# Kernel optimization log

Measured on AMD Instinct MI355X. Metric: run time of the kernel, lower is better.

The kernel has to match this reference:

```python
import jax, jax.numpy as jnp
import numpy as np
from jax import lax

B, T, NI = 1024, 16, 11

def skew(v):  # [...,3,1] -> [...,3,3]
    x, y, z = v[..., 0, 0], v[..., 1, 0], v[..., 2, 0]
    o = jnp.zeros_like(x)
    return jnp.stack([jnp.stack([o, -z, y], -1),
                      jnp.stack([z, o, -x], -1),
                      jnp.stack([-y, x, o], -1)], -2)

def exp_SO3(phi):  # [...,3,1] -> [...,3,3] (Rodrigues, safe small-angle)
    t2 = jnp.sum(phi * phi, axis=(-2, -1))[..., None, None]
    small = t2 < 1e-8
    t2s = jnp.where(small, 1.0, t2)
    t = jnp.sqrt(t2s)
    A = jnp.where(small, 1.0 - t2 / 6.0, jnp.sin(t) / t)
    Bc = jnp.where(small, 0.5 - t2 / 24.0, (1.0 - jnp.cos(t)) / t2s)
    K = skew(phi)
    return jnp.eye(3, dtype=phi.dtype) + A * K + Bc * (K @ K)

def log_SO3(C):  # [...,3,3] -> [...,3,1]
    tr = jnp.trace(C, axis1=-2, axis2=-1)[..., None, None]
    c = jnp.clip((tr - 1.0) * 0.5, -1.0 + 1e-7, 1.0 - 1e-7)
    t = jnp.arccos(c)
    small = t < 1e-4
    s = jnp.where(small, 1.0, jnp.sin(t))
    coef = jnp.where(small, 0.5 + t * t / 12.0, t / (2.0 * s))
    S = coef * (C - jnp.swapaxes(C, -1, -2))
    return jnp.stack([S[..., 2, 1], S[..., 0, 2], S[..., 1, 0]], -1)[..., None]

def J_left_inv(phi):  # inverse left Jacobian of SO(3)
    t2 = jnp.sum(phi * phi, axis=(-2, -1))[..., None, None]
    small = t2 < 1e-8
    t2s = jnp.where(small, 1.0, t2)
    t = jnp.sqrt(t2s)
    coef = jnp.where(small, 1.0 / 12.0,
                     1.0 / t2s - (1.0 + jnp.cos(t)) / (2.0 * t * jnp.sin(t)))
    K = skew(phi)
    return jnp.eye(3, dtype=phi.dtype) - 0.5 * K + coef * (K @ K)

def decode(s):
    b = s.shape[0]
    return (s[:, 0:3].reshape(b, 3, 1), s[:, 3:12].reshape(b, 3, 3),
            s[:, 12:15].reshape(b, 3, 1), s[:, 15:18].reshape(b, 3, 1),
            s[:, 18:21].reshape(b, 3, 1), s[:, 21:24].reshape(b, 3, 1),
            s[:, 24].reshape(b, 1, 1))

def encode(g, C, r, v, bw, ba, lambd):
    b = g.shape[0]
    return jnp.concatenate([g.reshape(b, 3), C.reshape(b, 9), r.reshape(b, 3),
                            v.reshape(b, 3), bw.reshape(b, 3), ba.reshape(b, 3),
                            lambd.reshape(b, 1)], -1)

def force_sym(M):
    u = jnp.triu(M)
    return u + jnp.swapaxes(u, -1, -2) * (1.0 - jnp.eye(M.shape[-1], dtype=M.dtype))

def predict_one_step(t_acc, C_acc, r_acc, v_acc, dt, g_k, v_k, bw_k, ba_k, covar, gyro, accel, Rimu):
    b = dt.shape[0]
    dt2 = dt * dt
    w = gyro - bw_k
    w_sk = skew(w)
    C_T = jnp.swapaxes(C_acc, -1, -2)
    a = accel - ba_k
    v = C_T @ (v_k - g_k * t_acc + v_acc)
    v_sk = skew(v)
    I3 = jnp.eye(3, dtype=dt.dtype)
    E = exp_SO3(dt * w)
    E_T = jnp.swapaxes(E, -1, -2)
    F = jnp.zeros((b, 19, 19), dt.dtype)
    F = F.at[:, 3:6, 3:6].set(-w_sk)
    F = F.at[:, 3:6, 12:15].set(-I3)
    F = F.at[:, 6:9, 3:6].set(-(C_acc @ v_sk))
    F = F.at[:, 6:9, 9:12].set(C_acc)
    F = F.at[:, 9:12, 0:3].set(-C_T)
    F = F.at[:, 9:12, 3:6].set(-skew(C_T @ g_k))
    F = F.at[:, 9:12, 9:12].set(-w_sk)
    F = F.at[:, 9:12, 12:15].set(-v_sk)
    F = F.at[:, 9:12, 15:18].set(-I3)
    G = jnp.zeros((b, 19, 12), dt.dtype)
    G = G.at[:, 3:6, 0:3].set(-I3)
    G = G.at[:, 9:12, 0:3].set(-v_sk)
    G = G.at[:, 9:12, 6:9].set(-I3)
    G = G.at[:, 12:15, 3:6].set(I3)
    G = G.at[:, 15:18, 9:12].set(I3)
    Phi = jnp.eye(19, dtype=dt.dtype) + F * dt + 0.5 * (F @ F) * dt2
    Phi = Phi.at[:, 6:9, 12:15].set(0.0)
    Phi = Phi.at[:, 3:6, 3:6].set(E_T)
    Phi = Phi.at[:, 9:12, 9:12].set(E_T)
    PhiG = Phi @ G
    Q = (PhiG @ Rimu @ jnp.swapaxes(PhiG, -1, -2)) * dt
    covar = force_sym(Phi @ covar @ jnp.swapaxes(Phi, -1, -2) + Q)
    r_acc = r_acc + v_acc * dt + 0.5 * (C_acc @ (dt2 * a))
    v_acc = v_acc + C_acc @ (dt * a)
    C_acc = C_acc @ E
    t_acc = t_acc + dt
    return t_acc, C_acc, r_acc, v_acc, covar

def predict(imu_meas, Rimu, prev_state, prev_covar):
    b = imu_meas.shape[0]
    dtype = prev_covar.dtype
    g_k, _, _, v_k, bw_k, ba_k, lambd = decode(prev_state)
    u = jnp.array([1.0] * 3 + [0.0] * 6 + [1.0] * 10, dtype)
    covar = prev_covar * (u[:, None] * u[None, :])  # U P U^T with diagonal U
    t = imu_meas[..., 0]
    gyro = imu_meas[..., 1:4][..., None]
    accel = imu_meas[..., 4:7][..., None]
    dt = (t[:, 1:] - t[:, :-1])[..., None, None]
    init = (jnp.zeros((b, 1, 1), dtype),
            jnp.tile(jnp.eye(3, dtype=dtype), (b, 1, 1)),
            jnp.zeros((b, 3, 1), dtype), jnp.zeros((b, 3, 1), dtype), covar)
    xs = (jnp.swapaxes(dt, 0, 1), jnp.swapaxes(gyro[:, :-1], 0, 1), jnp.swapaxes(accel[:, :-1], 0, 1))
    def step(c, x):
        t_acc, C_acc, r_acc, v_acc, cov = c
        dt_, gy, ac = x
        return predict_one_step(t_acc, C_acc, r_acc, v_acc, dt_, g_k, v_k, bw_k, ba_k, cov, gy, ac, Rimu), None
    (t_acc, C_acc, r_acc, v_acc, cov), _ = lax.scan(step, init, xs)
    pred_state = encode(g_k, C_acc,
                        v_k * t_acc - 0.5 * g_k * t_acc * t_acc + r_acc,
                        jnp.swapaxes(C_acc, -1, -2) @ (v_k - g_k * t_acc + v_acc),
                        bw_k, ba_k, lambd)
    return pred_state, cov

def update(pred_state, pred_covar, vis_meas, vis_meas_covar):
    b = pred_state.shape[0]
    dtype = pred_state.dtype
    g_p, C_p, r_p, v_p, bw_p, ba_p, l_p = decode(pred_state)
    phi = log_SO3(C_p)
    residual = jnp.concatenate([vis_meas[:, 0:3] - phi, vis_meas[:, 3:6] - l_p * r_p], 1)
    H = jnp.zeros((b, 6, 19), dtype)
    H = H.at[:, 0:3, 3:6].set(-J_left_inv(-phi))
    H = H.at[:, 3:6, 6:9].set(-jnp.eye(3, dtype=dtype) * l_p)
    H = H.at[:, 3:6, 18:19].set(-r_p)
    H = -H
    H_T = jnp.swapaxes(H, -1, -2)
    S = H @ pred_covar @ H_T + vis_meas_covar
    K = pred_covar @ H_T @ jnp.linalg.inv(S)
    e = K @ residual
    est_covar = (jnp.eye(19, dtype=dtype) - K @ H) @ pred_covar
    est_state = encode(g_p + e[:, 0:3], C_p @ exp_SO3(e[:, 3:6]), r_p + e[:, 6:9],
                       v_p + e[:, 9:12], bw_p + e[:, 12:15], ba_p + e[:, 15:18],
                       l_p + e[:, 18:19])
    return est_state, est_covar

def composition(prev_pose, est_state, est_covar):
    b = est_state.shape[0]
    dtype = est_state.dtype
    g, C, r, v, bw, ba, lambd = decode(est_state)
    C_T = jnp.swapaxes(C, -1, -2)
    pose = jnp.tile(jnp.eye(4, dtype=dtype), (b, 1, 1))
    pose = pose.at[:, 0:3, 0:3].set(C_T @ prev_pose[:, 0:3, 0:3])
    pose = pose.at[:, 0:3, 3:4].set(C_T @ (prev_pose[:, 0:3, 3:4] - r))
    new_g = C_T @ g
    new_state = encode(new_g, C, r, v, bw, ba, lambd)
    U = jnp.tile(jnp.eye(19, dtype=dtype), (b, 1, 1))
    U = U.at[:, 0:3, 0:3].set(C_T)
    U = U.at[:, 0:3, 3:6].set(skew(new_g))
    new_covar = force_sym(U @ est_covar @ jnp.swapaxes(U, -1, -2))
    return pose, new_state, new_covar

def setup_inputs() -> dict:
    key = jax.random.key(0)
    k1, k2, k3 = jax.random.split(key, 3)
    dtype = jnp.float32
    times = jnp.broadcast_to(jnp.arange(NI, dtype=dtype) * 0.01, (B, T, NI))
    gyro = jax.random.normal(k1, (B, T, NI, 3), dtype) * 0.05
    accel = jax.random.normal(k2, (B, T, NI, 3), dtype) * 0.1
    imu_data = jnp.concatenate([times[..., None], gyro, accel], -1)  # [B,T,NI,7]
    imu_noise_covar = jnp.eye(12, dtype=dtype) * 1e-4
    prev_pose = jnp.tile(jnp.eye(4, dtype=dtype), (B, 1, 1))
    g0 = jnp.array([0.0, 0.0, 9.81], dtype)
    C0 = jnp.eye(3, dtype=dtype).reshape(9)
    prev_state = jnp.broadcast_to(
        jnp.concatenate([g0, C0, jnp.zeros(12, dtype), jnp.ones(1, dtype)]), (B, 25))
    prev_covar = jnp.tile(jnp.eye(19, dtype=dtype) * 1e-2, (B, 1, 1))
    vis_meas = jax.random.normal(k3, (B, T, 6, 1), dtype) * 0.01
    vis_meas_covar = jnp.tile(jnp.eye(6, dtype=dtype) * 1e-2, (B, T, 1, 1))
    T_imu_cam = jnp.tile(jnp.eye(4, dtype=dtype), (B, 1, 1))
    return dict(imu_data=imu_data, imu_noise_covar=imu_noise_covar, prev_pose=prev_pose,
                prev_state=prev_state, prev_covar=prev_covar, vis_meas=vis_meas,
                vis_meas_covar=vis_meas_covar, T_imu_cam=T_imu_cam)

def reference(imu_data, imu_noise_covar, prev_pose, prev_state, prev_covar, vis_meas, vis_meas_covar, T_imu_cam):
    num_timesteps = vis_meas.shape[1]
    poses, states, covars = [prev_pose], [prev_state], [prev_covar]
    for k in range(num_timesteps):
        ps, pc = predict(imu_data[:, k], imu_noise_covar, states[-1], covars[-1])
        es, ec = update(ps, pc, vis_meas[:, k], vis_meas_covar[:, k])
        npo, ns, nc = composition(poses[-1], es, ec)
        poses.append(npo); states.append(ns); covars.append(nc)
    return (jnp.stack(poses, 1), jnp.stack(states, 1), jnp.stack(covars, 1))
```

## Files before the change

### kernel.cpp

```cpp
#include <hip/hip_runtime.h>

#define NB 1024
#define NT 16
#define NIM 11
#define PIT 20
#define NTH 256
#define TPF 128

struct __align__(16) SharedBlob {
    float P0[19*PIT];
    float P1[19*PIT];
    float A9[9*PIT];
    float Dall[10][9*PIT];
    float W9[9*12];
    float Wr9[9*12];
    float Wu[19*12];
    float Mu[19*12];
    float T[3*PIT];
    float Rd[12];
    float Aug[2][84];
    float E[20];
    float vvs[10][4];
    float dts[12];
    unsigned short tri[192];
};

__device__ __forceinline__ float sel3(int i, float a, float b, float c){
    return i==0 ? a : (i==1 ? b : c);
}
__device__ __forceinline__ void skew3(float x, float y, float z, float K[9]) {
    K[0]=0.f;  K[1]=-z;   K[2]=y;
    K[3]=z;    K[4]=0.f;  K[5]=-x;
    K[6]=-y;   K[7]=x;    K[8]=0.f;
}
__device__ __forceinline__ void mm3(const float A[9], const float Bm[9], float C[9]) {
#pragma unroll
    for (int i=0;i<3;i++)
#pragma unroll
        for (int j=0;j<3;j++)
            C[i*3+j] = A[i*3+0]*Bm[0+j] + A[i*3+1]*Bm[3+j] + A[i*3+2]*Bm[6+j];
}
__device__ __forceinline__ void exp_SO3f(float p0, float p1, float p2, float R[9]) {
    float t2 = p0*p0+p1*p1+p2*p2;
    bool sm = t2 < 1e-8f;
    float t2s = sm ? 1.0f : t2;
    float t = sqrtf(t2s);
    float sn, cs; __sincosf(t, &sn, &cs);
    float A = sm ? (1.0f - t2*(1.0f/6.0f)) : (sn/t);
    float Bc = sm ? (0.5f - t2*(1.0f/24.0f)) : ((1.0f - cs)/t2s);
    float K[9]; skew3(p0,p1,p2,K);
    float K2[9]; mm3(K,K,K2);
#pragma unroll
    for (int i=0;i<9;i++) R[i] = A*K[i] + Bc*K2[i];
    R[0]+=1.f; R[4]+=1.f; R[8]+=1.f;
}
__device__ __forceinline__ void log_SO3(const float C[9], float p[3]) {
    float tr = C[0]+C[4]+C[8];
    float c = (tr-1.0f)*0.5f;
    c = fminf(fmaxf(c, -1.0f+1e-7f), 1.0f-1e-7f);
    float t = acosf(c);
    bool sm = t < 1e-4f;
    float s = sm ? 1.0f : sinf(t);
    float coef = sm ? (0.5f + t*t*(1.0f/12.0f)) : (t/(2.0f*s));
    p[0] = coef*(C[7]-C[5]);
    p[1] = coef*(C[2]-C[6]);
    p[2] = coef*(C[3]-C[1]);
}
__device__ __forceinline__ void J_left_inv(const float p[3], float J[9]) {
    float t2 = p[0]*p[0]+p[1]*p[1]+p[2]*p[2];
    bool sm = t2 < 1e-8f;
    float t2s = sm ? 1.0f : t2;
    float t = sqrtf(t2s);
    float coef = sm ? (1.0f/12.0f) : (1.0f/t2s - (1.0f+cosf(t))/(2.0f*t*sinf(t)));
    float K[9]; skew3(p[0],p[1],p[2],K);
    float K2[9]; mm3(K,K,K2);
#pragma unroll
    for (int i=0;i<9;i++) J[i] = -0.5f*K[i] + coef*K2[i];
    J[0]+=1.f; J[4]+=1.f; J[8]+=1.f;
}
__device__ __forceinline__ float dot19_rr(const float* a, const float* b){
    const float4* a4=(const float4*)a;
    const float4* b4=(const float4*)b;
    float s=0.f;
#pragma unroll
    for (int q=0;q<4;q++){
        float4 x=a4[q], y=b4[q];
        s += x.x*y.x + x.y*y.y + x.z*y.z + x.w*y.w;
    }
    s += a[16]*b[16]+a[17]*b[17]+a[18]*b[18];
    return s;
}
__device__ __forceinline__ float dot12_rr(const float* a, const float* b){
    const float4* a4=(const float4*)a;
    const float4* b4=(const float4*)b;
    float s=0.f;
#pragma unroll
    for (int q=0;q<3;q++){
        float4 x=a4[q], y=b4[q];
        s += x.x*y.x + x.y*y.y + x.z*y.z + x.w*y.w;
    }
    return s;
}

__global__ void __launch_bounds__(NTH, 2) kf_kernel(
    const float* __restrict__ imu_data,
    const float* __restrict__ Rimu,
    const float* __restrict__ prev_pose,
    const float* __restrict__ prev_state,
    const float* __restrict__ prev_covar,
    const float* __restrict__ vis_meas,
    const float* __restrict__ vis_covar,
    float* __restrict__ out_poses,
    float* __restrict__ out_states,
    float* __restrict__ out_covars)
{
    __shared__ SharedBlob SS[2];
    const int tid = threadIdx.x;
    const int f   = tid >> 7;
    const int t   = tid & (TPF-1);
    const int b   = blockIdx.x*2 + f;
    SharedBlob& S = SS[f];

    const float* pcv = prev_covar + (size_t)b*361;
    for (int e=t;e<361;e+=TPF){
        float v = pcv[e];
        int i=e/19, j=e%19;
        bool msk = (i>=3&&i<9)||(j>=3&&j<9);
        S.P0[i*PIT + j] = msk ? 0.f : v;
        out_covars[((size_t)b*17)*361 + e] = v;
    }
    for (int e=t;e<10*9*PIT;e+=TPF) S.Dall[0][e] = 0.f;
    if (t<12) S.Rd[t] = Rimu[t*12+t];
    if (t<16) out_poses[((size_t)b*17)*16 + t] = prev_pose[(size_t)b*16+t];
    if (t<25) out_states[((size_t)b*17)*25 + t] = prev_state[(size_t)b*25+t];
    for (int e=t;e<190;e+=TPF){
        int i=0, rem=e;
        while (rem >= 19-i){ rem -= 19-i; i++; }
        S.tri[e] = (unsigned short)((i<<5)|(i+rem));
    }

    const float* st = prev_state + (size_t)b*25;
    float g0=st[0], g1=st[1], g2=st[2];
    float vk0=st[15], vk1=st[16], vk2=st[17];
    float bw0=st[18], bw1=st[19], bw2=st[20];
    float ba0=st[21], ba1=st[22], ba2=st[23];
    float lam=st[24];
    const float* pp = prev_pose + (size_t)b*16;
    float pR[9] = {pp[0],pp[1],pp[2], pp[4],pp[5],pp[6], pp[8],pp[9],pp[10]};
    float pT0=pp[3], pT1=pp[7], pT2=pp[11];

    __syncthreads();

    for (int k=0;k<NT;k++){
        float Cc[9] = {1,0,0, 0,1,0, 0,0,1};
        float ra0=0,ra1=0,ra2=0, va0=0,va1=0,va2=0, tac=0;
        const float* imu = imu_data + ((size_t)b*NT + k)*NIM*7;

        for (int s=0;s<NIM-1;s++){
            const float* m0 = imu + s*7;
            float dt = m0[7] - m0[0];
            float w0=m0[1]-bw0, w1=m0[2]-bw1, w2=m0[3]-bw2;
            float a0=m0[4]-ba0, a1=m0[5]-ba1, a2=m0[6]-ba2;
            float u0=vk0-g0*tac+va0, u1=vk1-g1*tac+va1, u2=vk2-g2*tac+va2;
            float vv0=Cc[0]*u0+Cc[3]*u1+Cc[6]*u2;
            float vv1=Cc[1]*u0+Cc[4]*u1+Cc[7]*u2;
            float vv2=Cc[2]*u0+Cc[5]*u1+Cc[8]*u2;
            float ct0=Cc[0]*g0+Cc[3]*g1+Cc[6]*g2;
            float ct1=Cc[1]*g0+Cc[4]*g1+Cc[7]*g2;
            float ct2=Cc[2]*g0+Cc[5]*g1+Cc[8]*g2;
            float Em[9]; exp_SO3f(dt*w0, dt*w1, dt*w2, Em);
            float hdt2 = 0.5f*dt*dt;

            if (t<27){
                int r=t/9, ii=(t%9)/3, jj=t%3;
                float dij = (ii==jj)?1.f:0.f;
                int o = ii*PIT + jj;
                float* Dp = S.Dall[s];
                if (r==0){
                    float eJ0=sel3(jj,Em[0],Em[3],Em[6]), eJ1=sel3(jj,Em[1],Em[4],Em[7]), eJ2=sel3(jj,Em[2],Em[5],Em[8]);
                    float EmTIJ = sel3(ii,eJ0,eJ1,eJ2);
                    float wcJ0=sel3(jj,0.f,-w2,w1), wcJ1=sel3(jj,w2,0.f,-w0), wcJ2=sel3(jj,-w1,w0,0.f);
                    float wskIJ = sel3(ii,wcJ0,wcJ1,wcJ2);
                    Dp[o+3]  = EmTIJ - dij;
                    Dp[o+12] = -dt*dij + hdt2*wskIJ;
                } else if (r==1){
                    float cI0=sel3(ii,Cc[0],Cc[3],Cc[6]), cI1=sel3(ii,Cc[1],Cc[4],Cc[7]), cI2=sel3(ii,Cc[2],Cc[5],Cc[8]);
                    float cJ0=sel3(jj,Cc[0],Cc[3],Cc[6]), cJ1=sel3(jj,Cc[1],Cc[4],Cc[7]), cJ2=sel3(jj,Cc[2],Cc[5],Cc[8]);
                    float ccJ0=sel3(jj,Cc[0],Cc[1],Cc[2]), ccJ1=sel3(jj,Cc[3],Cc[4],Cc[5]), ccJ2=sel3(jj,Cc[6],Cc[7],Cc[8]);
                    float CIJ = sel3(ii,ccJ0,ccJ1,ccJ2);
                    float vcJ0=sel3(jj,0.f,-vv2,vv1), vcJ1=sel3(jj,vv2,0.f,-vv0), vcJ2=sel3(jj,-vv1,vv0,0.f);
                    float tcJ0=sel3(jj,0.f,-ct2,ct1), tcJ1=sel3(jj,ct2,0.f,-ct0), tcJ2=sel3(jj,-ct1,ct0,0.f);
                    float wcJ0=sel3(jj,0.f,-w2,w1), wcJ1=sel3(jj,w2,0.f,-w0), wcJ2=sel3(jj,-w1,w0,0.f);
                    float CCtIJ  = cI0*cJ0 + cI1*cJ1 + cI2*cJ2;
                    float CvskIJ = cI0*vcJ0 + cI1*vcJ1 + cI2*vcJ2;
                    float Cv0 =  cI1*vv2 - cI2*vv1;
                    float Cv1 = -cI0*vv2 + cI2*vv0;
                    float Cv2 =  cI0*vv1 - cI1*vv0;
                    float CvwIJ = Cv0*wcJ0 + Cv1*wcJ1 + Cv2*wcJ2;
                    float CctIJ = cI0*tcJ0 + cI1*tcJ1 + cI2*tcJ2;
                    float CwIJ  = cI0*wcJ0 + cI1*wcJ1 + cI2*wcJ2;
                    Dp[3*PIT + o + 0]  = -hdt2*CCtIJ;
                    Dp[3*PIT + o + 3]  = -dt*CvskIJ + hdt2*(CvwIJ - CctIJ);
                    Dp[3*PIT + o + 9]  =  dt*CIJ - hdt2*CwIJ;
                    Dp[3*PIT + o + 15] = -hdt2*CIJ;
                } else {
                    float cJ0=sel3(jj,Cc[0],Cc[3],Cc[6]), cJ1=sel3(jj,Cc[1],Cc[4],Cc[7]), cJ2=sel3(jj,Cc[2],Cc[5],Cc[8]);
                    float CTIJ = sel3(ii,cJ0,cJ1,cJ2);
                    float eJ0=sel3(jj,Em[0],Em[3],Em[6]), eJ1=sel3(jj,Em[1],Em[4],Em[7]), eJ2=sel3(jj,Em[2],Em[5],Em[8]);
                    float EmTIJ = sel3(ii,eJ0,eJ1,eJ2);
                    float wrI0=sel3(ii,0.f,w2,-w1), wrI1=sel3(ii,-w2,0.f,w0), wrI2=sel3(ii,w1,-w0,0.f);
                    float wcJ0=sel3(jj,0.f,-w2,w1), wcJ1=sel3(jj,w2,0.f,-w0), wcJ2=sel3(jj,-w1,w0,0.f);
                    float wskIJ = sel3(ii,wcJ0,wcJ1,wcJ2);
                    float vcJ0=sel3(jj,0.f,-vv2,vv1), vcJ1=sel3(jj,vv2,0.f,-vv0), vcJ2=sel3(jj,-vv1,vv0,0.f);
                    float vskIJ = sel3(ii,vcJ0,vcJ1,vcJ2);
                    float trI0=sel3(ii,0.f,ct2,-ct1), trI1=sel3(ii,-ct2,0.f,ct0), trI2=sel3(ii,ct1,-ct0,0.f);
                    float tcJ0=sel3(jj,0.f,-ct2,ct1), tcJ1=sel3(jj,ct2,0.f,-ct0), tcJ2=sel3(jj,-ct1,ct0,0.f);
                    float ctskIJ = sel3(ii,tcJ0,tcJ1,tcJ2);
                    float wCtIJ = wrI0*cJ0 + wrI1*cJ1 + wrI2*cJ2;
                    float ctwIJ = trI0*wcJ0 + trI1*wcJ1 + trI2*wcJ2;
                    float wctIJ = wrI0*tcJ0 + wrI1*tcJ1 + wrI2*tcJ2;
                    float wvIJ  = wrI0*vcJ0 + wrI1*vcJ1 + wrI2*vcJ2;
                    Dp[6*PIT + o + 0]  = -dt*CTIJ + hdt2*wCtIJ;
                    Dp[6*PIT + o + 3]  = -dt*ctskIJ + hdt2*(ctwIJ + wctIJ);
                    Dp[6*PIT + o + 9]  = EmTIJ - dij;
                    Dp[6*PIT + o + 12] = -dt*vskIJ + hdt2*(ctskIJ + wvIJ);
                    Dp[6*PIT + o + 15] = -dt*dij + hdt2*wskIJ;
                }
            }
            if (t<3) S.vvs[s][t] = sel3(t, vv0, vv1, vv2);
            if (t==3) S.dts[s] = dt;

            float d2 = dt*dt;
            float e0=d2*a0, e1=d2*a1, e2=d2*a2;
            ra0 += va0*dt + 0.5f*(Cc[0]*e0+Cc[1]*e1+Cc[2]*e2);
            ra1 += va1*dt + 0.5f*(Cc[3]*e0+Cc[4]*e1+Cc[5]*e2);
            ra2 += va2*dt + 0.5f*(Cc[6]*e0+Cc[7]*e1+Cc[8]*e2);
            float da0=dt*a0, da1=dt*a1, da2=dt*a2;
            va0 += Cc[0]*da0+Cc[1]*da1+Cc[2]*da2;
            va1 += Cc[3]*da0+Cc[4]*da1+Cc[5]*da2;
            va2 += Cc[6]*da0+Cc[7]*da1+Cc[8]*da2;
            float Cn[9]; mm3(Cc, Em, Cn);
#pragma unroll
            for (int q=0;q<9;q++) Cc[q]=Cn[q];
            tac += dt;
        }
        __syncthreads();

        for (int s=0;s<NIM-1;s++){
            float* Pc = (s&1) ? S.P1 : S.P0;
            float* Pn = (s&1) ? S.P0 : S.P1;
            const float* Ds = S.Dall[s];
            float vv0=S.vvs[s][0], vv1=S.vvs[s][1], vv2=S.vvs[s][2];
            float dt = S.dts[s];

            for (int e=t;e<279;e+=TPF){
                if (e<171){
                    int i=e/19, j=e%19;
                    const float* Dr = &Ds[i*PIT];
                    float s2 = Pc[(3+i)*PIT+j]
                             + Dr[0]*Pc[0*PIT+j]+Dr[1]*Pc[1*PIT+j]+Dr[2]*Pc[2*PIT+j]
                             + Dr[3]*Pc[3*PIT+j]+Dr[4]*Pc[4*PIT+j]+Dr[5]*Pc[5*PIT+j]
                             + Dr[9]*Pc[9*PIT+j]+Dr[10]*Pc[10*PIT+j]+Dr[11]*Pc[11*PIT+j]
                             + Dr[12]*Pc[12*PIT+j]+Dr[13]*Pc[13*PIT+j]+Dr[14]*Pc[14*PIT+j]
                             + Dr[15]*Pc[15*PIT+j]+Dr[16]*Pc[16*PIT+j]+Dr[17]*Pc[17*PIT+j];
                    S.A9[i*PIT+j]=s2;
                } else {
                    int e2=e-171; int i=e2/12, j=e2%12;
                    const float* Dr = &Ds[i*PIT];
                    int ri = 3+i;
                    float val;
                    if (j<3){
                        float v0j = sel3(j, 0.f, -vv2,  vv1);
                        float v1j = sel3(j, vv2,  0.f, -vv0);
                        float v2j = sel3(j,-vv1,  vv0,  0.f);
                        val = -((ri==3+j)?1.f:0.f) - Dr[3+j]
                              - (((ri==9 )?1.f:0.f)+Dr[9 ])*v0j
                              - (((ri==10)?1.f:0.f)+Dr[10])*v1j
                              - (((ri==11)?1.f:0.f)+Dr[11])*v2j;
                    } else if (j<6) val = Dr[9+j];
                    else if (j<9) val = -(((ri==j+3)?1.f:0.f) + Dr[j+3]);
                    else val = Dr[6+j];
                    S.W9[i*12+j]=val;
                    S.Wr9[i*12+j]=val*S.Rd[j];
                }
            }
            __syncthreads();

            for (int e=t;e<190;e+=TPF){
                int tt=S.tri[e]; int i=tt>>5, j=tt&31;
                const float* Ai = (i>=3 && i<12) ? &S.A9[(i-3)*PIT] : &Pc[i*PIT];
                float val = Ai[j];
                if (j>=3 && j<12) val += dot19_rr(Ai, &Ds[(j-3)*PIT]);
                if (i>=3){
                    if (j<12) val += dt*dot12_rr(&S.Wr9[(i-3)*12], &S.W9[(j-3)*12]);
                    else if (i<12){
                        if (j<15) val += dt*S.Wr9[(i-3)*12 + (j-9)];
                        else if (j<18) val += dt*S.Wr9[(i-3)*12 + (j-6)];
                    } else if (i==j){
                        if (i<15) val += dt*S.Rd[i-9];
                        else if (i<18) val += dt*S.Rd[i-6];
                    }
                }
                Pn[i*PIT+j]=val; Pn[j*PIT+i]=val;
            }
            __syncthreads();
        }

        float t2a = tac*tac;
        float rp0 = vk0*tac - 0.5f*g0*t2a + ra0;
        float rp1 = vk1*tac - 0.5f*g1*t2a + ra1;
        float rp2 = vk2*tac - 0.5f*g2*t2a + ra2;
        float u0=vk0-g0*tac+va0, u1=vk1-g1*tac+va1, u2=vk2-g2*tac+va2;
        float vpr0=Cc[0]*u0+Cc[3]*u1+Cc[6]*u2;
        float vpr1=Cc[1]*u0+Cc[4]*u1+Cc[7]*u2;
        float vpr2=Cc[2]*u0+Cc[5]*u1+Cc[8]*u2;

        float phi[3]; log_SO3(Cc, phi);
        float nphi[3]={-phi[0],-phi[1],-phi[2]};
        float Jli[9]; J_left_inv(nphi, Jli);
        const float* vm = vis_meas + ((size_t)b*NT+k)*6;
        float res0=vm[0]-phi[0], res1=vm[1]-phi[1], res2=vm[2]-phi[2];
        float res3=vm[3]-lam*rp0, res4=vm[4]-lam*rp1, res5=vm[5]-lam*rp2;

        if (t<114){
            int i=t/6, j=t%6;
            float val;
            if (j<3){
                float jr0 = sel3(j, Jli[0], Jli[3], Jli[6]);
                float jr1 = sel3(j, Jli[1], Jli[4], Jli[7]);
                float jr2 = sel3(j, Jli[2], Jli[5], Jli[8]);
                val = S.P0[i*PIT+3]*jr0 + S.P0[i*PIT+4]*jr1 + S.P0[i*PIT+5]*jr2;
            } else {
                float rsel = sel3(j-3, rp0, rp1, rp2);
                val = lam*S.P0[i*PIT+6+(j-3)] + rsel*S.P0[i*PIT+18];
            }
            S.Wu[i*12+j]=val;
        }
        __syncthreads();
        const float* vmc = vis_covar + ((size_t)b*NT+k)*36;
        if (t<84){
            int i=t/14, c=t%14;
            float val;
            if (c<6){
                float hp;
                if (i<3){
                    float jr0 = sel3(i, Jli[0], Jli[3], Jli[6]);
                    float jr1 = sel3(i, Jli[1], Jli[4], Jli[7]);
                    float jr2 = sel3(i, Jli[2], Jli[5], Jli[8]);
                    hp = jr0*S.Wu[3*12+c]+jr1*S.Wu[4*12+c]+jr2*S.Wu[5*12+c];
                } else {
                    float rsel = sel3(i-3, rp0, rp1, rp2);
                    hp = lam*S.Wu[(3+i)*12+c] + rsel*S.Wu[18*12+c];
                }
                val = hp + vmc[i*6+c];
            } else val = ((c-6)==i)?1.f:0.f;
            S.Aug[0][i*14+c]=val;
        }
        __syncthreads();
        if (t<64){
            int i0=t/14, c0=t%14;
            int e1=t+64, i1=e1/14, c1=e1%14;
            bool h1 = e1<84;
            int cur=0;
#pragma unroll
            for (int kk=0;kk<6;kk++){
                const float* Ac = S.Aug[cur];
                float* An = S.Aug[cur^1];
                float rpv = 1.0f/Ac[kk*14+kk];
                float piv0 = Ac[kk*14+c0]*rpv;
                float nv0 = (i0==kk)? piv0 : (Ac[i0*14+c0] - Ac[i0*14+kk]*piv0);
                float nv1 = 0.f;
                if (h1){
                    float piv1 = Ac[kk*14+c1]*rpv;
                    nv1 = (i1==kk)? piv1 : (Ac[i1*14+c1] - Ac[i1*14+kk]*piv1);
                }
                An[i0*14+c0]=nv0;
                if (h1) An[i1*14+c1]=nv1;
                cur^=1;
                __builtin_amdgcn_wave_barrier();
            }
        }
        __syncthreads();
        if (t<114){
            int i=t/6, j=t%6;
            float s2=0.f;
#pragma unroll
            for (int m=0;m<6;m++) s2 += S.Wu[i*12+m]*S.Aug[0][m*14+6+j];
            S.Mu[i*12+j]=s2;
        }
        __syncthreads();
        for (int e=t;e<133;e+=TPF){
            int i=e/7, c=e%7;
            float val;
            if (c<3){
                float jc0 = sel3(c, Jli[0], Jli[1], Jli[2]);
                float jc1 = sel3(c, Jli[3], Jli[4], Jli[5]);
                float jc2 = sel3(c, Jli[6], Jli[7], Jli[8]);
                val = S.Mu[i*12+0]*jc0 + S.Mu[i*12+1]*jc1 + S.Mu[i*12+2]*jc2;
            }
            else if (c<6) val = S.Mu[i*12+c]*lam;
            else val = S.Mu[i*12+3]*rp0 + S.Mu[i*12+4]*rp1 + S.Mu[i*12+5]*rp2;
            S.Wu[i*12+c]=val;
        }
        if (t<19){
            S.E[t] = S.Mu[t*12+0]*res0 + S.Mu[t*12+1]*res1 + S.Mu[t*12+2]*res2
                   + S.Mu[t*12+3]*res3 + S.Mu[t*12+4]*res4 + S.Mu[t*12+5]*res5;
        }
        __syncthreads();
        for (int e=t;e<361;e+=TPF){
            int i=e/19, j=e%19;
            float s2 = S.P0[i*PIT+j];
#pragma unroll
            for (int c=0;c<6;c++) s2 -= S.Wu[i*12+c]*S.P0[(3+c)*PIT+j];
            s2 -= S.Wu[i*12+6]*S.P0[18*PIT+j];
            S.P1[i*PIT+j]=s2;
        }
        float ev[19];
#pragma unroll
        for (int q=0;q<19;q++) ev[q]=S.E[q];
        g0+=ev[0]; g1+=ev[1]; g2+=ev[2];
        float dE[9]; exp_SO3f(ev[3], ev[4], ev[5], dE);
        float Ce[9]; mm3(Cc,dE,Ce);
        float re0=rp0+ev[6], re1=rp1+ev[7], re2=rp2+ev[8];
        float vE0=vpr0+ev[9], vE1=vpr1+ev[10], vE2=vpr2+ev[11];
        bw0+=ev[12]; bw1+=ev[13]; bw2+=ev[14];
        ba0+=ev[15]; ba1+=ev[16]; ba2+=ev[17];
        lam+=ev[18];
        float gn0=Ce[0]*g0+Ce[3]*g1+Ce[6]*g2;
        float gn1=Ce[1]*g0+Ce[4]*g1+Ce[7]*g2;
        float gn2=Ce[2]*g0+Ce[5]*g1+Ce[8]*g2;
        float Rn[9];
#pragma unroll
        for (int i=0;i<3;i++)
#pragma unroll
            for (int j=0;j<3;j++)
                Rn[i*3+j] = Ce[0*3+i]*pR[0*3+j] + Ce[1*3+i]*pR[1*3+j] + Ce[2*3+i]*pR[2*3+j];
        float dv0=pT0-re0, dv1=pT1-re1, dv2=pT2-re2;
        float Tn0=Ce[0]*dv0+Ce[3]*dv1+Ce[6]*dv2;
        float Tn1=Ce[1]*dv0+Ce[4]*dv1+Ce[7]*dv2;
        float Tn2=Ce[2]*dv0+Ce[5]*dv1+Ce[8]*dv2;
        __syncthreads();
        if (t<57){
            int i=t/19, j=t%19;
            float c0 = sel3(i, Ce[0], Ce[1], Ce[2]);
            float c1 = sel3(i, Ce[3], Ce[4], Ce[5]);
            float c2 = sel3(i, Ce[6], Ce[7], Ce[8]);
            float gs0 = sel3(i, 0.f,  gn2, -gn1);
            float gs1 = sel3(i, -gn2, 0.f,  gn0);
            float gs2 = sel3(i, gn1, -gn0,  0.f);
            float val = c0*S.P1[0*PIT+j] + c1*S.P1[1*PIT+j] + c2*S.P1[2*PIT+j]
                      + gs0*S.P1[3*PIT+j] + gs1*S.P1[4*PIT+j] + gs2*S.P1[5*PIT+j];
            S.T[i*PIT+j]=val;
        }
        __syncthreads();
        size_t obase = (size_t)b*17 + (size_t)(k+1);
        for (int e=t;e<190;e+=TPF){
            int tt=S.tri[e]; int i=tt>>5, j=tt&31;
            float val;
            if (j<3){
                float c0 = sel3(j, Ce[0], Ce[1], Ce[2]);
                float c1 = sel3(j, Ce[3], Ce[4], Ce[5]);
                float c2 = sel3(j, Ce[6], Ce[7], Ce[8]);
                float gs0 = sel3(j, 0.f,  gn2, -gn1);
                float gs1 = sel3(j, -gn2, 0.f,  gn0);
                float gs2 = sel3(j, gn1, -gn0,  0.f);
                val = S.T[i*PIT+0]*c0 + S.T[i*PIT+1]*c1 + S.T[i*PIT+2]*c2
                    + S.T[i*PIT+3]*gs0 + S.T[i*PIT+4]*gs1 + S.T[i*PIT+5]*gs2;
            } else {
                val = (i<3) ? S.T[i*PIT+j] : S.P1[i*PIT+j];
            }
            bool msk = (i>=3&&i<9)||(j>=3&&j<9);
            float pv = msk ? 0.f : val;
            S.P0[i*PIT+j]=pv; S.P0[j*PIT+i]=pv;
            out_covars[obase*361 + i*19 + j] = val;
            if (i!=j) out_covars[obase*361 + j*19 + i] = val;
        }
        if (t==0){
            float* po = out_poses + obase*16;
            po[0]=Rn[0]; po[1]=Rn[1]; po[2]=Rn[2];  po[3]=Tn0;
            po[4]=Rn[3]; po[5]=Rn[4]; po[6]=Rn[5];  po[7]=Tn1;
            po[8]=Rn[6]; po[9]=Rn[7]; po[10]=Rn[8]; po[11]=Tn2;
            po[12]=0.f; po[13]=0.f; po[14]=0.f; po[15]=1.f;
            float* so = out_states + obase*25;
            so[0]=gn0; so[1]=gn1; so[2]=gn2;
#pragma unroll
            for (int q=0;q<9;q++) so[3+q]=Ce[q];
            so[12]=re0; so[13]=re1; so[14]=re2;
            so[15]=vE0; so[16]=vE1; so[17]=vE2;
            so[18]=bw0; so[19]=bw1; so[20]=bw2;
            so[21]=ba0; so[22]=ba1; so[23]=ba2;
            so[24]=lam;
        }
        g0=gn0; g1=gn1; g2=gn2;
        vk0=vE0; vk1=vE1; vk2=vE2;
#pragma unroll
        for (int q=0;q<9;q++) pR[q]=Rn[q];
        pT0=Tn0; pT1=Tn1; pT2=Tn2;
        __syncthreads();
    }
}

extern "C" void kernel_launch(void* const* d_in, const int* in_sizes, int n_in,
                              void* d_out, int out_size, void* d_ws, size_t ws_size,
                              hipStream_t stream) {
    const float* imu    = (const float*)d_in[0];
    const float* Rimu   = (const float*)d_in[1];
    const float* ppose  = (const float*)d_in[2];
    const float* pstate = (const float*)d_in[3];
    const float* pcov   = (const float*)d_in[4];
    const float* vm     = (const float*)d_in[5];
    const float* vmc    = (const float*)d_in[6];
    float* out = (float*)d_out;
    float* out_poses  = out;
    float* out_states = out + (size_t)NB*17*16;
    float* out_covars = out + (size_t)NB*17*16 + (size_t)NB*17*25;
    hipLaunchKernelGGL(kf_kernel, dim3(NB/2), dim3(NTH), 0, stream,
        imu, Rimu, ppose, pstate, pcov, vm, vmc, out_poses, out_states, out_covars);
}
```

Baseline: 676.0 us.

## Hoist W construction into the propagation loop and split covariance work per wave

The per-step W/Wr matrices are now built in the first propagation loop by wave 0 and stored for all steps. They use a sqrt(Rd) symmetric scaling, so a single array serves both dot-product operands. In the covariance recursion the A9 product and the upper-triangle update are split between the two waves along their data dependencies, which replaces one block-wide __syncthreads per step with wave-local barriers. The trade-off is more shared memory (10 stored W matrices) and an uneven work split between waves. It also assumes Dall[s] is visible to wave 0 without a block barrier, and that the Rd entries are non-negative for sqrt.

```diff
diff --git a/kernel.cpp b/kernel.cpp
--- a/kernel.cpp
+++ b/kernel.cpp
@@ -12,15 +12,14 @@
     float P1[19*PIT];
     float A9[9*PIT];
     float Dall[10][9*PIT];
-    float W9[9*12];
-    float Wr9[9*12];
+    float Wsall[10][9*12];
     float Wu[19*12];
     float Mu[19*12];
     float T[3*PIT];
     float Rd[12];
+    float sqRd[12];
     float Aug[2][84];
     float E[20];
-    float vvs[10][4];
     float dts[12];
     unsigned short tri[192];
 };
@@ -120,6 +119,8 @@
     const int t   = tid & (TPF-1);
     const int b   = blockIdx.x*2 + f;
     SharedBlob& S = SS[f];
+    const int w = t >> 6;
+    const int l = t & 63;
 
     const float* pcv = prev_covar + (size_t)b*361;
     for (int e=t;e<361;e+=TPF){
@@ -130,7 +131,7 @@
         out_covars[((size_t)b*17)*361 + e] = v;
     }
     for (int e=t;e<10*9*PIT;e+=TPF) S.Dall[0][e] = 0.f;
-    if (t<12) S.Rd[t] = Rimu[t*12+t];
+    if (t<12){ float rv = Rimu[t*12+t]; S.Rd[t]=rv; S.sqRd[t]=sqrtf(rv); }
     if (t<16) out_poses[((size_t)b*17)*16 + t] = prev_pose[(size_t)b*16+t];
     if (t<25) out_states[((size_t)b*17)*25 + t] = prev_state[(size_t)b*25+t];
     for (int e=t;e<190;e+=TPF){
@@ -227,46 +228,16 @@
                     Dp[6*PIT + o + 15] = -dt*dij + hdt2*wskIJ;
                 }
             }
-            if (t<3) S.vvs[s][t] = sel3(t, vv0, vv1, vv2);
             if (t==3) S.dts[s] = dt;
-
-            float d2 = dt*dt;
-            float e0=d2*a0, e1=d2*a1, e2=d2*a2;
-            ra0 += va0*dt + 0.5f*(Cc[0]*e0+Cc[1]*e1+Cc[2]*e2);
-            ra1 += va1*dt + 0.5f*(Cc[3]*e0+Cc[4]*e1+Cc[5]*e2);
-            ra2 += va2*dt + 0.5f*(Cc[6]*e0+Cc[7]*e1+Cc[8]*e2);
-            float da0=dt*a0, da1=dt*a1, da2=dt*a2;
-            va0 += Cc[0]*da0+Cc[1]*da1+Cc[2]*da2;
-            va1 += Cc[3]*da0+Cc[4]*da1+Cc[5]*da2;
-            va2 += Cc[6]*da0+Cc[7]*da1+Cc[8]*da2;
-            float Cn[9]; mm3(Cc, Em, Cn);
-#pragma unroll
-            for (int q=0;q<9;q++) Cc[q]=Cn[q];
-            tac += dt;
-        }
-        __syncthreads();
-
-        for (int s=0;s<NIM-1;s++){
-            float* Pc = (s&1) ? S.P1 : S.P0;
-            float* Pn = (s&1) ? S.P0 : S.P1;
-            const float* Ds = S.Dall[s];
-            float vv0=S.vvs[s][0], vv1=S.vvs[s][1], vv2=S.vvs[s][2];
-            float dt = S.dts[s];
-
-            for (int e=t;e<279;e+=TPF){
-                if (e<171){
-                    int i=e/19, j=e%19;
-                    const float* Dr = &Ds[i*PIT];
-                    float s2 = Pc[(3+i)*PIT+j]
-                             + Dr[0]*Pc[0*PIT+j]+Dr[1]*Pc[1*PIT+j]+Dr[2]*Pc[2*PIT+j]
-                             + Dr[3]*Pc[3*PIT+j]+Dr[4]*Pc[4*PIT+j]+Dr[5]*Pc[5*PIT+j]
-                             + Dr[9]*Pc[9*PIT+j]+Dr[10]*Pc[10*PIT+j]+Dr[11]*Pc[11*PIT+j]
-                             + Dr[12]*Pc[12*PIT+j]+Dr[13]*Pc[13*PIT+j]+Dr[14]*Pc[14*PIT+j]
-                             + Dr[15]*Pc[15*PIT+j]+Dr[16]*Pc[16*PIT+j]+Dr[17]*Pc[17*PIT+j];
-                    S.A9[i*PIT+j]=s2;
-                } else {
-                    int e2=e-171; int i=e2/12, j=e2%12;
-                    const float* Dr = &Ds[i*PIT];
+            if (w==0){
+                __builtin_amdgcn_wave_barrier();
+                asm volatile("s_waitcnt lgkmcnt(0)" ::: "memory");
+                __builtin_amdgcn_wave_barrier();
+                float* Wp = S.Wsall[s];
+                const float* Dp2 = S.Dall[s];
+                for (int e=l;e<108;e+=64){
+                    int i=e/12, j=e%12;
+                    const float* Dr = &Dp2[i*PIT];
                     int ri = 3+i;
                     float val;
                     if (j<3){
@@ -280,22 +251,60 @@
                     } else if (j<6) val = Dr[9+j];
                     else if (j<9) val = -(((ri==j+3)?1.f:0.f) + Dr[j+3]);
                     else val = Dr[6+j];
-                    S.W9[i*12+j]=val;
-                    S.Wr9[i*12+j]=val*S.Rd[j];
+                    Wp[i*12+j] = val * S.sqRd[j];
                 }
             }
-            __syncthreads();
-
-            for (int e=t;e<190;e+=TPF){
-                int tt=S.tri[e]; int i=tt>>5, j=tt&31;
+
+            float d2 = dt*dt;
+            float e0=d2*a0, e1=d2*a1, e2=d2*a2;
+            ra0 += va0*dt + 0.5f*(Cc[0]*e0+Cc[1]*e1+Cc[2]*e2);
+            ra1 += va1*dt + 0.5f*(Cc[3]*e0+Cc[4]*e1+Cc[5]*e2);
+            ra2 += va2*dt + 0.5f*(Cc[6]*e0+Cc[7]*e1+Cc[8]*e2);
+            float da0=dt*a0, da1=dt*a1, da2=dt*a2;
+            va0 += Cc[0]*da0+Cc[1]*da1+Cc[2]*da2;
+            va1 += Cc[3]*da0+Cc[4]*da1+Cc[5]*da2;
+            va2 += Cc[6]*da0+Cc[7]*da1+Cc[8]*da2;
+            float Cn[9]; mm3(Cc, Em, Cn);
+#pragma unroll
+            for (int q=0;q<9;q++) Cc[q]=Cn[q];
+            tac += dt;
+        }
+        __syncthreads();
+
+        for (int s=0;s<NIM-1;s++){
+            float* Pc = (s&1) ? S.P1 : S.P0;
+            float* Pn = (s&1) ? S.P0 : S.P1;
+            const float* Ds = S.Dall[s];
+            const float* Wss = S.Wsall[s];
+            float dt = S.dts[s];
+
+            int aBeg = (w==0)?0:57, aEnd = (w==0)?57:171;
+            for (int e=aBeg+l;e<aEnd;e+=64){
+                int i=e/19, j=e%19;
+                const float* Dr = &Ds[i*PIT];
+                float s2 = Pc[(3+i)*PIT+j]
+                         + Dr[0]*Pc[0*PIT+j]+Dr[1]*Pc[1*PIT+j]+Dr[2]*Pc[2*PIT+j]
+                         + Dr[3]*Pc[3*PIT+j]+Dr[4]*Pc[4*PIT+j]+Dr[5]*Pc[5*PIT+j]
+                         + Dr[9]*Pc[9*PIT+j]+Dr[10]*Pc[10*PIT+j]+Dr[11]*Pc[11*PIT+j]
+                         + Dr[12]*Pc[12*PIT+j]+Dr[13]*Pc[13*PIT+j]+Dr[14]*Pc[14*PIT+j]
+                         + Dr[15]*Pc[15*PIT+j]+Dr[16]*Pc[16*PIT+j]+Dr[17]*Pc[17*PIT+j];
+                S.A9[i*PIT+j]=s2;
+            }
+            __builtin_amdgcn_wave_barrier();
+            asm volatile("s_waitcnt lgkmcnt(0)" ::: "memory");
+            __builtin_amdgcn_wave_barrier();
+
+            int tBase = (w==0)?0:99, tCnt = (w==0)?99:91;
+            for (int e2=l;e2<tCnt;e2+=64){
+                int tt=S.tri[tBase+e2]; int i=tt>>5, j=tt&31;
                 const float* Ai = (i>=3 && i<12) ? &S.A9[(i-3)*PIT] : &Pc[i*PIT];
                 float val = Ai[j];
                 if (j>=3 && j<12) val += dot19_rr(Ai, &Ds[(j-3)*PIT]);
                 if (i>=3){
-                    if (j<12) val += dt*dot12_rr(&S.Wr9[(i-3)*12], &S.W9[(j-3)*12]);
+                    if (j<12) val += dt*dot12_rr(&Wss[(i-3)*12], &Wss[(j-3)*12]);
                     else if (i<12){
-                        if (j<15) val += dt*S.Wr9[(i-3)*12 + (j-9)];
-                        else if (j<18) val += dt*S.Wr9[(i-3)*12 + (j-6)];
+                        if (j<15) val += dt*Wss[(i-3)*12 + (j-9)]*S.sqRd[j-9];
+                        else if (j<18) val += dt*Wss[(i-3)*12 + (j-6)]*S.sqRd[j-6];
                     } else if (i==j){
                         if (i<15) val += dt*S.Rd[i-9];
                         else if (i<18) val += dt*S.Rd[i-6];
```

After: 633.2 us. 6.3% less time.
